# Optimization experiments

Measured on AMD Instinct MI355X. Metric: run time of the kernel, lower is better.

Reference implementation:

```python
import jax, jax.numpy as jnp
import numpy as np

INPUT_DIM = 10              # number of binary covariates in x
N = 2_000_000               # batch size
C = 2 ** (INPUT_DIM + 1)    # 2048 (t, x) combinations, one Linear(1,1) each


def setup_inputs() -> dict:
    key = jax.random.key(0)
    kx, kt, ky, kw, kb = jax.random.split(key, 5)
    x = jax.random.randint(kx, (N, INPUT_DIM), 0, 2).astype(jnp.float32)  # binary covariates
    t = jax.random.randint(kt, (N, 1), 0, 2).astype(jnp.float32)          # binary treatment
    y = jax.random.normal(ky, (N, 1), dtype=jnp.float32)                  # outcome
    # Per-combination Linear(1,1): weight w[i] and bias b[i] for q_z_dummies[i]
    w = jax.random.normal(kw, (C,), dtype=jnp.float32) * 0.5
    b = jax.random.normal(kb, (C,), dtype=jnp.float32) * 0.5
    return {"x": x, "t": t, "y": y, "w": w, "b": b}


def reference(x, t, y, w, b):
    # The torch loop sums (w_i*y + b_i) * [exact match of (t, x) with combination i].
    # Exactly one combination matches per row, so this equals a gather at the
    # combination index. itertools.product([0,1], repeat=d+1) orders bits
    # (t, x_0, ..., x_{d-1}) with the FIRST bit most significant.
    powers = (2 ** jnp.arange(INPUT_DIM - 1, -1, -1)).astype(x.dtype)      # [d]
    idx = (t[:, 0] * (2 ** INPUT_DIM) + x @ powers).astype(jnp.int32)      # [N]
    z_logits = y * w[idx][:, None] + b[idx][:, None]                       # [N, 1]
    # Original returns (z_mu=0, z_var=0, z_logits) in binary mode; z_logits is
    # the only tensor output.
    return z_logits
```

## Files before the change

### kernel.cpp

```cpp
#include <hip/hip_runtime.h>
#include <hip/hip_bf16.h>


#define INPUT_DIM 10

__global__ __launch_bounds__(256) void enc_kernel(
    const float* __restrict__ x,
    const float* __restrict__ t,
    const float* __restrict__ y,
    const float* __restrict__ w,
    const float* __restrict__ b,
    float* __restrict__ out,
    int n)
{
    int i = blockIdx.x * blockDim.x + threadIdx.x;
    if (i >= n) return;

    const float2* xr = (const float2*)(x + (size_t)i * INPUT_DIM);
    float2 a0 = xr[0];
    float2 a1 = xr[1];
    float2 a2 = xr[2];
    float2 a3 = xr[3];
    float2 a4 = xr[4];

    int idx = ((int)t[i]) << 10;
    idx |= ((int)a0.x << 9) | ((int)a0.y << 8)
         | ((int)a1.x << 7) | ((int)a1.y << 6)
         | ((int)a2.x << 5) | ((int)a2.y << 4)
         | ((int)a3.x << 3) | ((int)a3.y << 2)
         | ((int)a4.x << 1) | ((int)a4.y);

    out[i] = fmaf(y[i], w[idx], b[idx]);
}

extern "C" void kernel_launch(void* const* d_in, const int* in_sizes, int n_in,
                              void* d_out, int out_size, void* d_ws, size_t ws_size,
                              hipStream_t stream) {
    const float* x = (const float*)d_in[0];
    const float* t = (const float*)d_in[1];
    const float* y = (const float*)d_in[2];
    const float* w = (const float*)d_in[3];
    const float* b = (const float*)d_in[4];
    float* out = (float*)d_out;

    int n = out_size;
    int block = 256;
    int grid = (n + block - 1) / block;
    enc_kernel<<<grid, block, 0, stream>>>(x, t, y, w, b, out, n);
}
```

Baseline: 132.5 us.

## Stage x rows through LDS with coalesced float4 loads, 512 rows per block

Each block now cooperatively copies 512 rows of x into shared memory using fully coalesced float4 loads, then each thread builds its index from LDS, handling two rows per thread. This replaces the strided 40-byte-per-thread float2 loads, which made poorly coalesced global accesses. The index is computed with float FMAs instead of int conversions and shifts. The cost is a block-wide barrier and 20KB of LDS per block, which may limit occupancy.

```diff
diff --git a/kernel.cpp b/kernel.cpp
--- a/kernel.cpp
+++ b/kernel.cpp
@@ -3,6 +3,7 @@
 
 
 #define INPUT_DIM 10
+#define ROWS_PER_BLOCK 512
 
 __global__ __launch_bounds__(256) void enc_kernel(
     const float* __restrict__ x,
@@ -13,24 +14,38 @@
     float* __restrict__ out,
     int n)
 {
-    int i = blockIdx.x * blockDim.x + threadIdx.x;
-    if (i >= n) return;
+    __shared__ __align__(16) float xs[ROWS_PER_BLOCK * INPUT_DIM];
 
-    const float2* xr = (const float2*)(x + (size_t)i * INPUT_DIM);
-    float2 a0 = xr[0];
-    float2 a1 = xr[1];
-    float2 a2 = xr[2];
-    float2 a3 = xr[3];
-    float2 a4 = xr[4];
+    const int base = blockIdx.x * ROWS_PER_BLOCK;
+    const int rows = (n - base < ROWS_PER_BLOCK) ? (n - base) : ROWS_PER_BLOCK;
+    const int dw_valid = rows * INPUT_DIM;
+    const float* gx = x + (size_t)base * INPUT_DIM;
 
-    int idx = ((int)t[i]) << 10;
-    idx |= ((int)a0.x << 9) | ((int)a0.y << 8)
-         | ((int)a1.x << 7) | ((int)a1.y << 6)
-         | ((int)a2.x << 5) | ((int)a2.y << 4)
-         | ((int)a3.x << 3) | ((int)a3.y << 2)
-         | ((int)a4.x << 1) | ((int)a4.y);
+#pragma unroll
+    for (int k = 0; k < 5; ++k) {
+        int d = (threadIdx.x + k * 256) * 4;
+        if (d + 4 <= dw_valid) {
+            *(float4*)&xs[d] = *(const float4*)&gx[d];
+        } else if (d < dw_valid) {
+            for (int j = d; j < dw_valid; ++j) xs[j] = gx[j];
+        }
+    }
+    __syncthreads();
 
-    out[i] = fmaf(y[i], w[idx], b[idx]);
+    for (int r = threadIdx.x; r < rows; r += 256) {
+        const int g = base + r;
+        const float* xr = &xs[r * INPUT_DIM];
+
+        float s0 = fmaf(xr[0], 512.f, t[g] * 1024.f);
+        float s1 = fmaf(xr[1], 256.f, xr[2] * 128.f);
+        float s2 = fmaf(xr[3],  64.f, xr[4] *  32.f);
+        float s3 = fmaf(xr[5],  16.f, xr[6] *   8.f);
+        float s4 = fmaf(xr[7],   4.f, xr[8] *   2.f);
+        float s5 = s4 + xr[9];
+        int idx = (int)((s0 + s1) + (s2 + s3) + s5);
+
+        out[g] = fmaf(y[g], w[idx], b[idx]);
+    }
 }
 
 extern "C" void kernel_launch(void* const* d_in, const int* in_sizes, int n_in,
@@ -44,7 +59,6 @@
     float* out = (float*)d_out;
 
     int n = out_size;
-    int block = 256;
-    int grid = (n + block - 1) / block;
-    enc_kernel<<<grid, block, 0, stream>>>(x, t, y, w, b, out, n);
+    int grid = (n + ROWS_PER_BLOCK - 1) / ROWS_PER_BLOCK;
+    enc_kernel<<<grid, 256, 0, stream>>>(x, t, y, w, b, out, n);
 }
```

Result: slower. 136.5 us (+3.1%).
